# Optimization experiments

Hardware: AMD Instinct MI355X
Metric: run time of the kernel (lower is better)

Reference implementation:

```python
import jax, jax.numpy as jnp
import numpy as np

N = 100000   # nodes
E = 5000000  # edges (avg degree 50)
H = 16       # hidden dim


def gcn_conv(x, edge_index, edge_weight, W, b, num_nodes):
    """PyG GCNConv with edge weights: add self-loops (weight 1), symmetric
    normalization deg^-1/2 * w * deg^-1/2, linear transform, scatter-add."""
    row, col = edge_index[0], edge_index[1]  # source j -> target i
    loop = jnp.arange(num_nodes, dtype=edge_index.dtype)
    row = jnp.concatenate([row, loop])
    col = jnp.concatenate([col, loop])
    w = jnp.concatenate([edge_weight, jnp.ones((num_nodes,), edge_weight.dtype)])
    deg = jax.ops.segment_sum(w, col, num_segments=num_nodes)
    dinv = jnp.where(deg > 0, jax.lax.rsqrt(jnp.where(deg > 0, deg, 1.0)), 0.0)
    norm = dinv[row] * w * dinv[col]               # [E+N]
    h = x @ W                                      # [N, out]
    msg = norm[:, None] * h[row]                   # gather + scale
    out = jax.ops.segment_sum(msg, col, num_segments=num_nodes)  # scatter-add
    return out + b


def setup_inputs() -> dict:
    key = jax.random.key(0)
    k = jax.random.split(key, 7)
    x = jax.random.normal(k[0], (N, 1), dtype=jnp.float32)
    edge_index = jax.random.randint(k[1], (2, E), 0, N, dtype=jnp.int32)
    edge_attr = jax.random.uniform(k[2], (E,), dtype=jnp.float32)
    W1 = jax.random.normal(k[3], (1, H), dtype=jnp.float32) * (1.0 / np.sqrt(1.0))
    b1 = jnp.zeros((H,), dtype=jnp.float32)
    W2 = jax.random.normal(k[4], (H, 1), dtype=jnp.float32) * (1.0 / np.sqrt(H))
    b2 = jnp.zeros((1,), dtype=jnp.float32)
    return {"x": x, "edge_index": edge_index, "edge_attr": edge_attr,
            "W1": W1, "b1": b1, "W2": W2, "b2": b2}


def reference(x, edge_index, edge_attr, W1, b1, W2, b2):
    h = gcn_conv(x, edge_index, edge_attr, W1, b1, N)
    h = jax.nn.relu(h)
    out = gcn_conv(h, edge_index, edge_attr, W2, b2, N)
    return out
```

## Files before the change

kernel.cpp:

```cpp
#include <hip/hip_runtime.h>

#define THREADS 256
#define BSHIFT  12
#define BSIZE   4096
#define MAXNB   32
#define M       32
#define EPB     2048
#define EPT     (EPB / THREADS)

__global__ void k_count(const int* __restrict__ col, int* __restrict__ cnt,
                        int E, int nb) {
    __shared__ int hist[MAXNB];
    int t = threadIdx.x;
    if (t < nb) hist[t] = 0;
    __syncthreads();
    int base = blockIdx.x * EPB;
#pragma unroll
    for (int k = 0; k < EPT; ++k) {
        int e = base + t + k * THREADS;
        if (e < E) atomicAdd(&hist[col[e] >> BSHIFT], 1);
    }
    __syncthreads();
    if (t < nb && hist[t]) atomicAdd(&cnt[t], hist[t]);
}

__global__ void k_scan(const int* __restrict__ cnt, int* __restrict__ starts,
                       int* __restrict__ cur, int nb) {
    if (threadIdx.x == 0) {
        int s = 0;
        for (int b = 0; b < nb; ++b) { starts[b] = s; cur[b] = s; s += cnt[b]; }
        starts[nb] = s;
    }
}

__global__ void k_scatter(const int* __restrict__ row, const int* __restrict__ col,
                          const float* __restrict__ w, int* __restrict__ cur,
                          int* __restrict__ packed, float* __restrict__ wrec,
                          int E, int nb) {
    __shared__ int hist[MAXNB];
    __shared__ int rbase[MAXNB];
    int t = threadIdx.x;
    if (t < nb) hist[t] = 0;
    __syncthreads();
    int base = blockIdx.x * EPB;
    int  b_[EPT], rk_[EPT], pk_[EPT];
    float w_[EPT];
#pragma unroll
    for (int k = 0; k < EPT; ++k) {
        int e = base + t + k * THREADS;
        if (e < E) {
            int c = col[e];
            int b = c >> BSHIFT;
            b_[k]  = b;
            rk_[k] = atomicAdd(&hist[b], 1);
            pk_[k] = ((c & (BSIZE - 1)) << 17) | row[e];
            w_[k]  = w[e];
        } else b_[k] = -1;
    }
    __syncthreads();
    if (t < nb) rbase[t] = hist[t] ? atomicAdd(&cur[t], hist[t]) : 0;
    __syncthreads();
#pragma unroll
    for (int k = 0; k < EPT; ++k) {
        if (b_[k] >= 0) {
            int pos = rbase[b_[k]] + rk_[k];
            packed[pos] = pk_[k];
            wrec[pos]   = w_[k];
        }
    }
}

__global__ void k_acc(const int* __restrict__ packed, const float* __restrict__ wrec,
                      const int* __restrict__ starts, const int* __restrict__ cnt,
                      const float* __restrict__ src, float* __restrict__ part) {
    __shared__ float acc[BSIZE];
    int b = blockIdx.x / M, m = blockIdx.x % M;
    for (int j = threadIdx.x; j < BSIZE; j += THREADS) acc[j] = 0.0f;
    __syncthreads();
    int s = starts[b], c = cnt[b];
    int chunk = (c + M - 1) / M;
    int lo = s + m * chunk;
    int hi = min(s + c, lo + chunk);
    for (int i = lo + threadIdx.x; i < hi; i += THREADS) {
        int   pk = packed[i];
        float v  = wrec[i];
        if (src) v *= src[pk & 0x1FFFF];
        atomicAdd(&acc[((unsigned)pk) >> 17], v);
    }
    __syncthreads();
    float* dst = part + (size_t)blockIdx.x * BSIZE;
    for (int j = threadIdx.x; j < BSIZE; j += THREADS) dst[j] = acc[j];
}

__device__ __forceinline__ float reduceM(const float* __restrict__ part, int n) {
    int b = n >> BSHIFT, ofs = n & (BSIZE - 1);
    const float* pp = part + (size_t)b * M * BSIZE + ofs;
    float s = 0.0f;
#pragma unroll
    for (int m = 0; m < M; ++m) s += pp[(size_t)m * BSIZE];
    return s;
}

__global__ void k_red_dinv(const float* __restrict__ part, const float* __restrict__ x,
                           float* __restrict__ dinv, float* __restrict__ p, int N) {
    int i = blockIdx.x * blockDim.x + threadIdx.x;
    if (i < N) {
        float d  = reduceM(part, i) + 1.0f;
        float di = rsqrtf(d);
        dinv[i] = di;
        p[i] = di * x[i];
    }
}

__global__ void k_red_mlp(const float* __restrict__ part, const float* __restrict__ dinv,
                          const float* __restrict__ p,
                          const float* __restrict__ W1, const float* __restrict__ b1,
                          const float* __restrict__ W2,
                          float* __restrict__ q, int N) {
    int i = blockIdx.x * blockDim.x + threadIdx.x;
    if (i < N) {
        float di = dinv[i];
        float s  = di * reduceM(part, i) + di * p[i];
        float acc = 0.0f;
#pragma unroll
        for (int k = 0; k < 16; ++k) {
            float h = fmaxf(s * W1[k] + b1[k], 0.0f);
            acc += h * W2[k];
        }
        q[i] = di * acc;
    }
}

__global__ void k_red_out(const float* __restrict__ part, const float* __restrict__ dinv,
                          const float* __restrict__ q, const float* __restrict__ b2,
                          float* __restrict__ out, int N) {
    int i = blockIdx.x * blockDim.x + threadIdx.x;
    if (i < N) {
        float di = dinv[i];
        out[i] = di * reduceM(part, i) + di * q[i] + b2[0];
    }
}

extern "C" void kernel_launch(void* const* d_in, const int* in_sizes, int n_in,
                              void* d_out, int out_size, void* d_ws, size_t ws_size,
                              hipStream_t stream) {
    const float* x  = (const float*)d_in[0];
    const int*   ei = (const int*)  d_in[1];
    const float* ew = (const float*)d_in[2];
    const float* W1 = (const float*)d_in[3];
    const float* b1 = (const float*)d_in[4];
    const float* W2 = (const float*)d_in[5];
    const float* b2 = (const float*)d_in[6];

    const int N = in_sizes[0];
    const int E = in_sizes[2];
    const int* row = ei;
    const int* col = ei + E;
    const int nb = (N + BSIZE - 1) >> BSHIFT;

    char* wsp = (char*)d_ws;
    int*   packed = (int*)wsp;                         wsp += (size_t)E * 4;
    float* wrec   = (float*)wsp;                       wsp += (size_t)E * 4;
    float* part   = (float*)wsp;                       wsp += (size_t)nb * M * BSIZE * 4;
    float* dinv   = (float*)wsp;                       wsp += (size_t)N * 4;
    float* p      = (float*)wsp;                       wsp += (size_t)N * 4;
    float* q      = (float*)wsp;                       wsp += (size_t)N * 4;
    int*   cnt    = (int*)wsp;                         wsp += MAXNB * 4;
    int*   starts = (int*)wsp;                         wsp += (MAXNB + 1) * 4;
    int*   cur    = (int*)wsp;

    float* out = (float*)d_out;

    const int eb = (E + EPB - 1) / EPB;
    const int nbk = (N + THREADS - 1) / THREADS;
    const int ab  = nb * M;

    hipMemsetAsync(cnt, 0, MAXNB * sizeof(int), stream);

    k_count  <<<eb, THREADS, 0, stream>>>(col, cnt, E, nb);
    k_scan   <<<1, 64, 0, stream>>>(cnt, starts, cur, nb);
    k_scatter<<<eb, THREADS, 0, stream>>>(row, col, ew, cur, packed, wrec, E, nb);

    k_acc     <<<ab, THREADS, 0, stream>>>(packed, wrec, starts, cnt, nullptr, part);
    k_red_dinv<<<nbk, THREADS, 0, stream>>>(part, x, dinv, p, N);

    k_acc    <<<ab, THREADS, 0, stream>>>(packed, wrec, starts, cnt, p, part);
    k_red_mlp<<<nbk, THREADS, 0, stream>>>(part, dinv, p, W1, b1, W2, q, N);

    k_acc    <<<ab, THREADS, 0, stream>>>(packed, wrec, starts, cnt, q, part);
    k_red_out<<<nbk, THREADS, 0, stream>>>(part, dinv, q, b2, out, N);
}
```

Baseline: 286.6 us.

## Stage scatter through LDS, pack edge records as int2, vectorize count loads

```diff
diff --git a/kernel.cpp b/kernel.cpp
--- a/kernel.cpp
+++ b/kernel.cpp
@@ -15,10 +15,21 @@
     if (t < nb) hist[t] = 0;
     __syncthreads();
     int base = blockIdx.x * EPB;
-#pragma unroll
-    for (int k = 0; k < EPT; ++k) {
-        int e = base + t + k * THREADS;
-        if (e < E) atomicAdd(&hist[col[e] >> BSHIFT], 1);
+    if (base + EPB <= E) {
+#pragma unroll
+        for (int k = 0; k < EPT / 4; ++k) {
+            int4 c = *(const int4*)(col + base + (t + k * THREADS) * 4);
+            atomicAdd(&hist[c.x >> BSHIFT], 1);
+            atomicAdd(&hist[c.y >> BSHIFT], 1);
+            atomicAdd(&hist[c.z >> BSHIFT], 1);
+            atomicAdd(&hist[c.w >> BSHIFT], 1);
+        }
+    } else {
+#pragma unroll
+        for (int k = 0; k < EPT; ++k) {
+            int e = base + t + k * THREADS;
+            if (e < E) atomicAdd(&hist[col[e] >> BSHIFT], 1);
+        }
     }
     __syncthreads();
     if (t < nb && hist[t]) atomicAdd(&cnt[t], hist[t]);
@@ -35,14 +46,16 @@
 
 __global__ void k_scatter(const int* __restrict__ row, const int* __restrict__ col,
                           const float* __restrict__ w, int* __restrict__ cur,
-                          int* __restrict__ packed, float* __restrict__ wrec,
-                          int E, int nb) {
-    __shared__ int hist[MAXNB];
-    __shared__ int rbase[MAXNB];
+                          int2* __restrict__ rec, int E, int nb) {
+    __shared__ int  hist[MAXNB];
+    __shared__ int  lofs[MAXNB + 1];
+    __shared__ int  rbase[MAXNB];
+    __shared__ int2 buf[EPB];
     int t = threadIdx.x;
     if (t < nb) hist[t] = 0;
     __syncthreads();
     int base = blockIdx.x * EPB;
+
     int  b_[EPT], rk_[EPT], pk_[EPT];
     float w_[EPT];
 #pragma unroll
@@ -58,19 +71,29 @@
         } else b_[k] = -1;
     }
     __syncthreads();
+    if (t == 0) {
+        int s = 0;
+        for (int b = 0; b < nb; ++b) { lofs[b] = s; s += hist[b]; }
+        lofs[nb] = s;
+    }
     if (t < nb) rbase[t] = hist[t] ? atomicAdd(&cur[t], hist[t]) : 0;
     __syncthreads();
 #pragma unroll
     for (int k = 0; k < EPT; ++k) {
-        if (b_[k] >= 0) {
-            int pos = rbase[b_[k]] + rk_[k];
-            packed[pos] = pk_[k];
-            wrec[pos]   = w_[k];
-        }
-    }
-}
-
-__global__ void k_acc(const int* __restrict__ packed, const float* __restrict__ wrec,
+        if (b_[k] >= 0)
+            buf[lofs[b_[k]] + rk_[k]] = make_int2(pk_[k], __float_as_int(w_[k]));
+    }
+    __syncthreads();
+    int total = lofs[nb];
+    for (int j = t; j < total; j += THREADS) {
+        int lo = 0, hi = nb;
+        while (hi - lo > 1) { int mid = (lo + hi) >> 1; if (lofs[mid] <= j) lo = mid; else hi = mid; }
+        rec[rbase[lo] + (j - lofs[lo])] = buf[j];
+    }
+}
+
+template <bool HAS_SRC>
+__global__ void k_acc(const int2* __restrict__ rec,
                       const int* __restrict__ starts, const int* __restrict__ cnt,
                       const float* __restrict__ src, float* __restrict__ part) {
     __shared__ float acc[BSIZE];
@@ -82,10 +105,10 @@
     int lo = s + m * chunk;
     int hi = min(s + c, lo + chunk);
     for (int i = lo + threadIdx.x; i < hi; i += THREADS) {
-        int   pk = packed[i];
-        float v  = wrec[i];
-        if (src) v *= src[pk & 0x1FFFF];
-        atomicAdd(&acc[((unsigned)pk) >> 17], v);
+        int2  r = rec[i];
+        float v = __int_as_float(r.y);
+        if (HAS_SRC) v *= src[r.x & 0x1FFFF];
+        atomicAdd(&acc[((unsigned)r.x) >> 17], v);
     }
     __syncthreads();
     float* dst = part + (size_t)blockIdx.x * BSIZE;
@@ -159,8 +182,7 @@
     const int nb = (N + BSIZE - 1) >> BSHIFT;
 
     char* wsp = (char*)d_ws;
-    int*   packed = (int*)wsp;                         wsp += (size_t)E * 4;
-    float* wrec   = (float*)wsp;                       wsp += (size_t)E * 4;
+    int2*  rec    = (int2*)wsp;                        wsp += (size_t)E * 8;
     float* part   = (float*)wsp;                       wsp += (size_t)nb * M * BSIZE * 4;
     float* dinv   = (float*)wsp;                       wsp += (size_t)N * 4;
     float* p      = (float*)wsp;                       wsp += (size_t)N * 4;
@@ -171,7 +193,7 @@
 
     float* out = (float*)d_out;
 
-    const int eb = (E + EPB - 1) / EPB;
+    const int eb  = (E + EPB - 1) / EPB;
     const int nbk = (N + THREADS - 1) / THREADS;
     const int ab  = nb * M;
 
@@ -179,14 +201,14 @@
 
     k_count  <<<eb, THREADS, 0, stream>>>(col, cnt, E, nb);
     k_scan   <<<1, 64, 0, stream>>>(cnt, starts, cur, nb);
-    k_scatter<<<eb, THREADS, 0, stream>>>(row, col, ew, cur, packed, wrec, E, nb);
-
-    k_acc     <<<ab, THREADS, 0, stream>>>(packed, wrec, starts, cnt, nullptr, part);
-    k_red_dinv<<<nbk, THREADS, 0, stream>>>(part, x, dinv, p, N);
-
-    k_acc    <<<ab, THREADS, 0, stream>>>(packed, wrec, starts, cnt, p, part);
-    k_red_mlp<<<nbk, THREADS, 0, stream>>>(part, dinv, p, W1, b1, W2, q, N);
-
-    k_acc    <<<ab, THREADS, 0, stream>>>(packed, wrec, starts, cnt, q, part);
-    k_red_out<<<nbk, THREADS, 0, stream>>>(part, dinv, q, b2, out, N);
-}
+    k_scatter<<<eb, THREADS, 0, stream>>>(row, col, ew, cur, rec, E, nb);
+
+    k_acc<false><<<ab, THREADS, 0, stream>>>(rec, starts, cnt, nullptr, part);
+    k_red_dinv  <<<nbk, THREADS, 0, stream>>>(part, x, dinv, p, N);
+
+    k_acc<true><<<ab, THREADS, 0, stream>>>(rec, starts, cnt, p, part);
+    k_red_mlp  <<<nbk, THREADS, 0, stream>>>(part, dinv, p, W1, b1, W2, q, N);
+
+    k_acc<true><<<ab, THREADS, 0, stream>>>(rec, starts, cnt, q, part);
+    k_red_out  <<<nbk, THREADS, 0, stream>>>(part, dinv, q, b2, out, N);
+}
```

After: 282.6 us. About the same (-1.4%).
